# Optimization experiments

Hardware: AMD Instinct MI355X
Metric: run time of the kernel (lower is better)

## Reference

```python
import jax, jax.numpy as jnp
import numpy as np

B = 4096        # number of (drug, disease) pair graphs
N_PER = 60      # nodes per subgraph (>= k)
N = B * N_PER   # 245760 total nodes
E = 2_000_000   # edges
F_IN = 64
L1, L2 = 32, 32 # latent_dim
K = 30          # sort-pool k
N_DRUG, N_DIS = 1024, 2048


def gcn_conv(x, src, dst, W, b, n):
    # PyG GCNConv (eval): h = XW; symmetric norm with self-loops; out = A_hat h + b
    h = x @ W
    deg = jax.ops.segment_sum(jnp.ones(src.shape[0], h.dtype), dst, num_segments=n) + 1.0
    dinv = deg ** -0.5
    msg = h[src] * (dinv[src] * dinv[dst])[:, None]
    out = jax.ops.segment_sum(msg, dst, num_segments=n)
    out = out + h * (dinv * dinv)[:, None]  # self-loop contribution
    return out + b


def dense_gcn(x, adj, W, b):
    # PyG DenseGCNConv: set diag to 1, D^-1/2 A D^-1/2, out = A_hat (x W) + b
    n = adj.shape[0]
    eye = jnp.eye(n, dtype=adj.dtype)
    a = adj * (1.0 - eye) + eye
    deg = a.sum(-1)
    dinv = jnp.where(deg > 0, deg ** -0.5, 0.0)
    a = dinv[:, None] * a * dinv[None, :]
    return a @ (x @ W) + b


def conv1d(x, w, b, stride):
    out = jax.lax.conv_general_dilated(x, w, (stride,), 'VALID',
                                       dimension_numbers=('NCH', 'OIH', 'NCH'))
    return out + b[None, :, None]


def setup_inputs():
    key = jax.random.key(0)
    ks = jax.random.split(key, 24)
    x = jax.random.normal(ks[0], (N, F_IN), jnp.float32)
    edge_index = jax.random.randint(ks[1], (2, E), 0, N)
    batch = jnp.repeat(jnp.arange(B), N_PER)
    node = jnp.stack([jax.random.randint(ks[2], (B,), 0, N_DRUG),
                      jax.random.randint(ks[3], (B,), 0, N_DIS)], axis=1)
    di_sim = jax.random.normal(ks[4], (N_DRUG, N_DRUG), jnp.float32)
    dr_sim = jax.random.normal(ks[5], (N_DIS, N_DIS), jnp.float32)
    drug_adj = jax.random.uniform(ks[6], (N_DRUG, N_DRUG), jnp.float32)
    dis_adj = jax.random.uniform(ks[7], (N_DIS, N_DIS), jnp.float32)
    p = jnp.array(0.5, jnp.float32)

    def w(k, shape):
        return jax.random.normal(k, shape, jnp.float32) * 0.05

    z = lambda s: jnp.zeros(s, jnp.float32)
    params = dict(
        W1=w(ks[8], (F_IN, L1)), b1=z((L1,)),
        W2=w(ks[9], (L1, L2)), b2=z((L2,)),
        W3=w(ks[10], (256, 64)), b3=z((64,)),
        W4=w(ks[11], (64, 16)), b4=z((16,)),
        lin_di_w=w(ks[12], (N_DRUG, 256)), lin_di_b=z((256,)),
        lin_dr_w=w(ks[13], (N_DIS, 256)), lin_dr_b=z((256,)),
        c1_w=w(ks[14], (128, 1, L1 + L2)), c1_b=z((128,)),
        c2_w=w(ks[15], (256, 128, 5)), c2_b=z((256,)),
        lin1_w=w(ks[16], (2816, 128)), lin1_b=z((128,)),
        lin2_w=w(ks[17], (128, 32)), lin2_b=z((32,)),
        bn_g=jnp.ones((32,), jnp.float32), bn_b=z((32,)),
        fcs_w=w(ks[18], (64, 32)), fcs_b=z((32,)),
        fcs2_w=w(ks[19], (32, 1)), fcs2_b=z((1,)),
    )
    return dict(x=x, edge_index=edge_index, batch=batch, node=node,
                di_sim=di_sim, dr_sim=dr_sim, drug_adj=drug_adj,
                dis_adj=dis_adj, p=p, **params)


def reference(x, edge_index, batch, node, di_sim, dr_sim, drug_adj, dis_adj, p,
              W1, b1, W2, b2, W3, b3, W4, b4,
              lin_di_w, lin_di_b, lin_dr_w, lin_dr_b,
              c1_w, c1_b, c2_w, c2_b, lin1_w, lin1_b, lin2_w, lin2_b,
              bn_g, bn_b, fcs_w, fcs_b, fcs2_w, fcs2_b):
    src, dst = edge_index[0], edge_index[1]
    # two GCN layers over the pair subgraphs
    x1 = jax.nn.relu(gcn_conv(x, src, dst, W1, b1, N))
    x2 = jax.nn.relu(gcn_conv(x1, src, dst, W2, b2, N))
    cs = jnp.concatenate([x1, x2], axis=1)       # [N, 64]
    D = cs.shape[1]
    # sort-pool: equal-size graphs, batch contiguous -> reshape and sort per graph
    xb = cs.reshape(B, N_PER, D)
    order = jnp.argsort(-xb[:, :, -1], axis=-1)  # descending by last channel
    xs = jnp.take_along_axis(xb, order[:, :, None], axis=1)[:, :K]  # [B, K, D]
    h = xs.reshape(B, 1, K * D)
    h = jax.nn.relu(conv1d(h, c1_w, c1_b, D))    # [B, 128, K]
    h = jax.lax.reduce_window(h, -jnp.inf, jax.lax.max, (1, 1, 2), (1, 1, 2), 'VALID')
    h = jax.nn.relu(conv1d(h, c2_w, c2_b, 1))    # [B, 256, 11]
    h = h.reshape(B, -1)                         # [B, 2816]
    h = jax.nn.relu(h @ lin1_w + lin1_b)
    h = h @ lin2_w + lin2_b
    h = jax.nn.relu(h * bn_g + bn_b)             # BatchNorm eval (mean 0, var 1)
    # dense similarity-graph branches (conv3/conv4 weights shared across branches)
    di_e = di_sim @ lin_di_w + lin_di_b
    di_f = jax.nn.relu(dense_gcn(di_e, drug_adj, W3, b3))
    di_o = jax.nn.relu(dense_gcn(di_f, drug_adj, W4, b4))
    di = di_o[node[:, 0]]
    dr_e = dr_sim @ lin_dr_w + lin_dr_b
    dr_f = jax.nn.relu(dense_gcn(dr_e, dis_adj, W3, b3))
    dr_o = jax.nn.relu(dense_gcn(dr_f, dis_adj, W4, b4))
    dr = dr_o[node[:, 1]]
    feat = jnp.concatenate([di, dr], axis=1)     # [B, 32]
    z = jnp.concatenate([h * p, feat * (1.0 - p)], axis=1)  # [B, 64]
    z = jax.nn.relu(z @ fcs_w + fcs_b)
    return (z @ fcs2_w + fcs2_b)[:, 0]
```

## Files before the change

### kernel.cpp

```cpp
#include <hip/hip_runtime.h>

#define NN 245760
#define NB 4096
#define NPER 60
#define NE 2000000
#define KSEL 30
#define NDRUG 1024
#define NDIS 2048
#define NBKT 480
#define CHUNK 2048
#define SEGCAP 4992

typedef unsigned short ushort_t;
typedef unsigned int uint_t;
using bf16x8 = __attribute__((ext_vector_type(8))) short;
using f32x4 = __attribute__((ext_vector_type(4))) float;

__device__ inline ushort_t f2bf(float f) {
    union { float f; unsigned int u; } v; v.f = f;
    unsigned int r = v.u + 0x7FFF + ((v.u >> 16) & 1);
    return (ushort_t)(r >> 16);
}

__global__ __launch_bounds__(256) void k_bscatter(const int* __restrict__ ei,
                                                  int* __restrict__ bfill,
                                                  uint_t* __restrict__ pairs) {
    __shared__ int hist[NBKT], fill[NBKT], gbase[NBKT];
    int t = threadIdx.x;
    long e0 = (long)blockIdx.x * CHUNK;
    int cnt = (int)min((long)CHUNK, (long)NE - e0);
    for (int i = t; i < NBKT; i += 256) { hist[i] = 0; fill[i] = 0; }
    __syncthreads();
    for (int i = t; i < cnt; i += 256)
        atomicAdd(&hist[ei[NE + e0 + i] >> 9], 1);
    __syncthreads();
    for (int i = t; i < NBKT; i += 256)
        if (hist[i]) gbase[i] = i * SEGCAP + atomicAdd(&bfill[i], hist[i]);
    __syncthreads();
    for (int i = t; i < cnt; i += 256) {
        int s = ei[e0 + i], d = ei[NE + e0 + i];
        int b = d >> 9;
        int pos = gbase[b] + atomicAdd(&fill[b], 1);
        if (pos < (b + 1) * SEGCAP)
            pairs[pos] = ((uint_t)s << 9) | (uint_t)(d & 511);
    }
}

__global__ __launch_bounds__(256) void k_bbuild(const uint_t* __restrict__ pairs,
                                                const int* __restrict__ bfill,
                                                int* __restrict__ csr,
                                                int* __restrict__ rowp,
                                                int* __restrict__ cntg,
                                                float* __restrict__ dinv) {
    __shared__ int hist[512], nbase[512], nfill[512], scanA[512], scanB[512];
    __shared__ int seg[SEGCAP];
    int t = threadIdx.x, b = blockIdx.x;
    int ebase = b * SEGCAP;
    int ecnt = bfill[b];
    if (ecnt > SEGCAP) ecnt = SEGCAP;
    for (int i = t; i < 512; i += 256) { hist[i] = 0; nfill[i] = 0; }
    __syncthreads();
    for (int i = t; i < ecnt; i += 256)
        atomicAdd(&hist[pairs[ebase + i] & 511], 1);
    __syncthreads();
    for (int i = t; i < 512; i += 256) scanA[i] = hist[i];
    __syncthreads();
    int* src = scanA; int* dst = scanB;
    for (int off = 1; off < 512; off <<= 1) {
        for (int i = t; i < 512; i += 256)
            dst[i] = src[i] + ((i >= off) ? src[i - off] : 0);
        __syncthreads();
        int* tmp = src; src = dst; dst = tmp;
    }
    for (int i = t; i < 512; i += 256) {
        int h = hist[i];
        int excl = src[i] - h;
        nbase[i] = excl;
        int n = (b << 9) + i;
        rowp[n] = ebase + excl;
        cntg[n] = h;
        dinv[n] = 1.0f / sqrtf((float)h + 1.0f);
    }
    __syncthreads();
    for (int i = t; i < ecnt; i += 256) {
        uint_t v = pairs[ebase + i];
        int ln = v & 511;
        int pos = nbase[ln] + atomicAdd(&nfill[ln], 1);
        if (pos < SEGCAP) seg[pos] = (int)(v >> 9);
    }
    __syncthreads();
    for (int i = t; i < ecnt; i += 256) csr[ebase + i] = seg[i];
}

__global__ __launch_bounds__(256) void k_xw(const float* __restrict__ A, const float* __restrict__ W,
                                            float* __restrict__ h, int K, int lda) {
    __shared__ float Xs[64][65];
    __shared__ float Ws[64][32];
    int t = threadIdx.x;
    int r0 = blockIdx.x * 64;
    int kq = K >> 2;
    for (int idx = t; idx < 64 * kq; idx += 256) {
        int row = idx / kq, q = idx % kq;
        float4 v = *(const float4*)(A + (long)(r0 + row) * lda + q * 4);
        Xs[row][q * 4 + 0] = v.x; Xs[row][q * 4 + 1] = v.y;
        Xs[row][q * 4 + 2] = v.z; Xs[row][q * 4 + 3] = v.w;
    }
    for (int idx = t; idx < K * 32; idx += 256) ((float*)Ws)[idx] = W[idx];
    __syncthreads();
    int r = (t >> 3) * 2, c = (t & 7) * 4;
    float4 acc0 = {0, 0, 0, 0}, acc1 = {0, 0, 0, 0};
    for (int k = 0; k < K; k++) {
        float x0 = Xs[r][k], x1 = Xs[r + 1][k];
        float4 w = *(const float4*)&Ws[k][c];
        acc0.x += x0 * w.x; acc0.y += x0 * w.y; acc0.z += x0 * w.z; acc0.w += x0 * w.w;
        acc1.x += x1 * w.x; acc1.y += x1 * w.y; acc1.z += x1 * w.z; acc1.w += x1 * w.w;
    }
    *(float4*)(h + (long)(r0 + r) * 32 + c) = acc0;
    *(float4*)(h + (long)(r0 + r + 1) * 32 + c) = acc1;
}

__global__ void k_gcn_agg(const float* __restrict__ h, const int* __restrict__ csr,
                          const int* __restrict__ rowp, const int* __restrict__ cnt,
                          const float* __restrict__ dinv, const float* __restrict__ bias,
                          float* __restrict__ out, int colofs) {
    int t = threadIdx.x;
    int l = t & 7, g = t >> 3;
    int wl = t & 63;
    int gbase = wl & ~7;
    int d = blockIdx.x * 32 + g;
    float dd = dinv[d];
    int start = rowp[d], c = cnt[d];
    float4 hv = *(const float4*)(h + (long)d * 32 + l * 4);
    float4 acc; acc.x = dd * hv.x; acc.y = dd * hv.y; acc.z = dd * hv.z; acc.w = dd * hv.w;
    int k = 0;
    while (k < c) {
        int nb = c - k; if (nb > 8) nb = 8;
        int sl = (l < nb) ? csr[start + k + l] : 0;
        int sj[8]; float ds[8]; float4 hj[8];
#pragma unroll
        for (int j = 0; j < 8; j++)
            sj[j] = __shfl(sl, gbase + j, 64);
#pragma unroll
        for (int j = 0; j < 8; j++)
            if (j < nb) ds[j] = dinv[sj[j]];
#pragma unroll
        for (int j = 0; j < 8; j++)
            if (j < nb) hj[j] = *(const float4*)(h + (long)sj[j] * 32 + l * 4);
#pragma unroll
        for (int j = 0; j < 8; j++) {
            if (j < nb) {
                acc.x += ds[j] * hj[j].x;
                acc.y += ds[j] * hj[j].y;
                acc.z += ds[j] * hj[j].z;
                acc.w += ds[j] * hj[j].w;
            }
        }
        k += nb;
    }
    float4 bv = *(const float4*)(bias + l * 4);
    float* op = out + (long)d * 64 + colofs + l * 4;
    op[0] = fmaxf(dd * acc.x + bv.x, 0.f);
    op[1] = fmaxf(dd * acc.y + bv.y, 0.f);
    op[2] = fmaxf(dd * acc.z + bv.z, 0.f);
    op[3] = fmaxf(dd * acc.w + bv.w, 0.f);
}

__global__ __launch_bounds__(256, 2) void k_conv1_mfma(const float* __restrict__ cs,
                                                       const int* __restrict__ sel,
                                                       const ushort_t* __restrict__ c1w16,
                                                       const float* __restrict__ c1b,
                                                       ushort_t* __restrict__ po16) {
    __shared__ ushort_t A_lds[128 * 72];
    __shared__ ushort_t B_lds[128 * 72];
    int t = threadIdx.x;
    int r0 = blockIdx.x * 128;
#pragma unroll
    for (int rnd = 0; rnd < 4; rnd++) {
        int idx = t + rnd * 256;
        int row = idx >> 3, seg = idx & 7;
        const float* src = cs + (long)sel[r0 + row] * 64 + seg * 8;
        float4 v0 = *(const float4*)src;
        float4 v1 = *(const float4*)(src + 4);
        ushort_t tmp[8] = {f2bf(v0.x), f2bf(v0.y), f2bf(v0.z), f2bf(v0.w),
                           f2bf(v1.x), f2bf(v1.y), f2bf(v1.z), f2bf(v1.w)};
        *(uint4*)&A_lds[row * 72 + seg * 8] = *(uint4*)tmp;
        *(uint4*)&B_lds[row * 72 + seg * 8] = *(const uint4*)(c1w16 + row * 64 + seg * 8);
    }
    __syncthreads();
    int wv = t >> 6, lane = t & 63;
    int wm = wv >> 1, wn = wv & 1;
    int lrow = lane & 15, lk = (lane >> 4) * 8, lr4 = (lane >> 4) * 4;
    f32x4 acc[4][4] = {};
#pragma unroll
    for (int kk = 0; kk < 2; kk++) {
        bf16x8 a[4], b[4];
#pragma unroll
        for (int f = 0; f < 4; f++) {
            a[f] = *(const bf16x8*)&A_lds[(wm * 64 + f * 16 + lrow) * 72 + kk * 32 + lk];
            b[f] = *(const bf16x8*)&B_lds[(wn * 64 + f * 16 + lrow) * 72 + kk * 32 + lk];
        }
#pragma unroll
        for (int i = 0; i < 4; i++)
#pragma unroll
            for (int j = 0; j < 4; j++)
                acc[i][j] = __builtin_amdgcn_mfma_f32_16x16x32_bf16(a[i], b[j], acc[i][j], 0, 0, 0);
    }
    __syncthreads();
    ushort_t* po_lds = A_lds;
#pragma unroll
    for (int fn = 0; fn < 4; fn++) {
        int col = wn * 64 + fn * 16 + lrow;
        float bb = c1b[col];
#pragma unroll
        for (int fm = 0; fm < 4; fm++) {
            int lrow2 = wm * 32 + fm * 8 + (lr4 >> 1);
            float v0 = fmaxf(acc[fm][fn][0] + bb, 0.f);
            float v1 = fmaxf(acc[fm][fn][1] + bb, 0.f);
            float v2 = fmaxf(acc[fm][fn][2] + bb, 0.f);
            float v3 = fmaxf(acc[fm][fn][3] + bb, 0.f);
            po_lds[lrow2 * 128 + col]       = f2bf(fmaxf(v0, v1));
            po_lds[(lrow2 + 1) * 128 + col] = f2bf(fmaxf(v2, v3));
        }
    }
    __syncthreads();
    uint4* dst = (uint4*)(po16 + (long)(r0 >> 1) * 128);
    const uint4* srcp = (const uint4*)po_lds;
#pragma unroll
    for (int i = 0; i < 4; i++) dst[t + i * 256] = srcp[t + i * 256];
}

__global__ __launch_bounds__(256, 2) void k_conv2_mfma(const ushort_t* __restrict__ pool16,
                                                       const ushort_t* __restrict__ w2colT,
                                                       ushort_t* __restrict__ act2,
                                                       const float* __restrict__ bias) {
    __shared__ ushort_t smem[2 * 128 * 72];
    ushort_t* A_lds = smem;
    ushort_t* B_lds = smem + 128 * 72;
    int t = threadIdx.x;
    int r0 = blockIdx.x * 128, c0 = blockIdx.y * 128;
    long abase[4]; const ushort_t* bptr[4]; int lofs[4];
#pragma unroll
    for (int rnd = 0; rnd < 4; rnd++) {
        int idx = t + rnd * 256;
        int row = idx >> 3, seg = idx & 7;
        int arow = r0 + row;
        int bb = arow / 11, tt2 = arow - bb * 11;
        abase[rnd] = (long)(bb * 15 + tt2) * 128 + seg * 8;
        bptr[rnd] = w2colT + (long)(c0 + row) * 640 + seg * 8;
        lofs[rnd] = row * 72 + seg * 8;
    }
    int wv = t >> 6, lane = t & 63;
    int wm = wv >> 1, wn = wv & 1;
    int lrow = lane & 15, lk = (lane >> 4) * 8, lr4 = (lane >> 4) * 4;
    f32x4 acc[4][4] = {};
    for (int k0 = 0; k0 < 640; k0 += 64) {
#pragma unroll
        for (int rnd = 0; rnd < 4; rnd++) {
            *(uint4*)&A_lds[lofs[rnd]] = *(const uint4*)(pool16 + abase[rnd] + k0);
            *(uint4*)&B_lds[lofs[rnd]] = *(const uint4*)(bptr[rnd] + k0);
        }
        __syncthreads();
#pragma unroll
        for (int kk = 0; kk < 2; kk++) {
            bf16x8 a[4], b[4];
#pragma unroll
            for (int f = 0; f < 4; f++) {
                a[f] = *(const bf16x8*)&A_lds[(wm * 64 + f * 16 + lrow) * 72 + kk * 32 + lk];
                b[f] = *(const bf16x8*)&B_lds[(wn * 64 + f * 16 + lrow) * 72 + kk * 32 + lk];
            }
#pragma unroll
            for (int i = 0; i < 4; i++)
#pragma unroll
                for (int j = 0; j < 4; j++)
                    acc[i][j] = __builtin_amdgcn_mfma_f32_16x16x32_bf16(a[i], b[j], acc[i][j], 0, 0, 0);
        }
        __syncthreads();
    }
    ushort_t* c_lds = smem;
#pragma unroll
    for (int fn = 0; fn < 4; fn++) {
        int col = wn * 64 + fn * 16 + lrow;
        float bv = bias[c0 + col];
#pragma unroll
        for (int fm = 0; fm < 4; fm++) {
            int lr = wm * 64 + fm * 16 + lr4;
#pragma unroll
            for (int j = 0; j < 4; j++)
                c_lds[(lr + j) * 128 + col] = f2bf(fmaxf(acc[fm][fn][j] + bv, 0.f));
        }
    }
    __syncthreads();
#pragma unroll
    for (int i = 0; i < 8; i++) {
        int idx = t + i * 256;
        int row = idx >> 4, q = idx & 15;
        *(uint4*)(act2 + (long)(r0 + row) * 256 + c0 + q * 8) = ((const uint4*)c_lds)[idx];
    }
}

__global__ __launch_bounds__(256, 2) void k_lin1_mfma(const ushort_t* __restrict__ A,
                                                      const ushort_t* __restrict__ Bm,
                                                      float* __restrict__ C) {
    __shared__ ushort_t A_lds[128 * 72];
    __shared__ ushort_t B_lds[128 * 72];
    int t = threadIdx.x;
    int r0 = blockIdx.x * 128;
    int kz = blockIdx.z;
    const ushort_t* ap[4]; const ushort_t* bp[4]; int lofs[4];
#pragma unroll
    for (int rnd = 0; rnd < 4; rnd++) {
        int idx = t + rnd * 256;
        int row = idx >> 3, seg = idx & 7;
        ap[rnd] = A + (long)(r0 + row) * 2816 + kz * 704 + seg * 8;
        bp[rnd] = Bm + (long)row * 2816 + kz * 704 + seg * 8;
        lofs[rnd] = row * 72 + seg * 8;
    }
    int wv = t >> 6, lane = t & 63;
    int wm = wv >> 1, wn = wv & 1;
    int lrow = lane & 15, lk = (lane >> 4) * 8, lr4 = (lane >> 4) * 4;
    f32x4 acc[4][4] = {};
    for (int k0 = 0; k0 < 704; k0 += 64) {
#pragma unroll
        for (int rnd = 0; rnd < 4; rnd++) {
            *(uint4*)&A_lds[lofs[rnd]] = *(const uint4*)(ap[rnd] + k0);
            *(uint4*)&B_lds[lofs[rnd]] = *(const uint4*)(bp[rnd] + k0);
        }
        __syncthreads();
#pragma unroll
        for (int kk = 0; kk < 2; kk++) {
            bf16x8 a[4], b[4];
#pragma unroll
            for (int f = 0; f < 4; f++) {
                a[f] = *(const bf16x8*)&A_lds[(wm * 64 + f * 16 + lrow) * 72 + kk * 32 + lk];
                b[f] = *(const bf16x8*)&B_lds[(wn * 64 + f * 16 + lrow) * 72 + kk * 32 + lk];
            }
#pragma unroll
            for (int i = 0; i < 4; i++)
#pragma unroll
                for (int j = 0; j < 4; j++)
                    acc[i][j] = __builtin_amdgcn_mfma_f32_16x16x32_bf16(a[i], b[j], acc[i][j], 0, 0, 0);
        }
        __syncthreads();
    }
#pragma unroll
    for (int fn = 0; fn < 4; fn++) {
        int col = wn * 64 + fn * 16 + lrow;
#pragma unroll
        for (int fm = 0; fm < 4; fm++) {
            int rowb = r0 + wm * 64 + fm * 16 + lr4;
#pragma unroll
            for (int j = 0; j < 4; j++)
                atomicAdd(&C[(long)(rowb + j) * 128 + col], acc[fm][fn][j]);
        }
    }
}

__global__ __launch_bounds__(256, 2) void k_de_mfma(
    const ushort_t* __restrict__ A0, const ushort_t* __restrict__ B0, float* __restrict__ C0,
    const float* __restrict__ bias0, int M0, int K0, int KS0,
    const ushort_t* __restrict__ A1, const ushort_t* __restrict__ B1, float* __restrict__ C1,
    const float* __restrict__ bias1, int M1, int K1, int KS1) {
    __shared__ ushort_t A_lds[128 * 72];
    __shared__ ushort_t B_lds[64 * 72];
    int z = blockIdx.z;
    const ushort_t* A; const ushort_t* Bm; float* C; const float* bias; int M, K, kz, KS;
    if (z < KS0) { A = A0; Bm = B0; C = C0; bias = bias0; M = M0; K = K0; kz = z; KS = KS0; }
    else { A = A1; Bm = B1; C = C1; bias = bias1; M = M1; K = K1; kz = z - KS0; KS = KS1; }
    int r0 = blockIdx.x * 128, c0 = blockIdx.y * 64;
    if (r0 >= M) return;
    int Kc = K / KS;
    int kb = kz * Kc;
    int t = threadIdx.x;
    const ushort_t* ap[4]; int alofs[4];
#pragma unroll
    for (int rnd = 0; rnd < 4; rnd++) {
        int idx = t + rnd * 256;
        int row = idx >> 3, seg = idx & 7;
        ap[rnd] = A + (long)(r0 + row) * K + kb + seg * 8;
        alofs[rnd] = row * 72 + seg * 8;
    }
    const ushort_t* bp[2]; int blofs[2];
#pragma unroll
    for (int rnd = 0; rnd < 2; rnd++) {
        int idx = t + rnd * 256;
        int row = idx >> 3, seg = idx & 7;
        bp[rnd] = Bm + (long)(c0 + row) * K + kb + seg * 8;
        blofs[rnd] = row * 72 + seg * 8;
    }
    int wv = t >> 6, lane = t & 63;
    int lrow = lane & 15, lk = (lane >> 4) * 8, lr4 = (lane >> 4) * 4;
    uint4 areg[4], breg[2];
#pragma unroll
    for (int rnd = 0; rnd < 4; rnd++) areg[rnd] = *(const uint4*)(ap[rnd]);
#pragma unroll
    for (int rnd = 0; rnd < 2; rnd++) breg[rnd] = *(const uint4*)(bp[rnd]);
    f32x4 acc[2][4] = {};
    for (int k0 = 0; k0 < Kc; k0 += 64) {
#pragma unroll
        for (int rnd = 0; rnd < 4; rnd++) *(uint4*)&A_lds[alofs[rnd]] = areg[rnd];
#pragma unroll
        for (int rnd = 0; rnd < 2; rnd++) *(uint4*)&B_lds[blofs[rnd]] = breg[rnd];
        __syncthreads();
        if (k0 + 64 < Kc) {
#pragma unroll
            for (int rnd = 0; rnd < 4; rnd++) areg[rnd] = *(const uint4*)(ap[rnd] + k0 + 64);
#pragma unroll
            for (int rnd = 0; rnd < 2; rnd++) breg[rnd] = *(const uint4*)(bp[rnd] + k0 + 64);
        }
#pragma unroll
        for (int kk = 0; kk < 2; kk++) {
            bf16x8 a[2], b[4];
#pragma unroll
            for (int f = 0; f < 2; f++)
                a[f] = *(const bf16x8*)&A_lds[(wv * 32 + f * 16 + lrow) * 72 + kk * 32 + lk];
#pragma unroll
            for (int f = 0; f < 4; f++)
                b[f] = *(const bf16x8*)&B_lds[(f * 16 + lrow) * 72 + kk * 32 + lk];
#pragma unroll
            for (int i = 0; i < 2; i++)
#pragma unroll
                for (int j = 0; j < 4; j++)
                    acc[i][j] = __builtin_amdgcn_mfma_f32_16x16x32_bf16(a[i], b[j], acc[i][j], 0, 0, 0);
        }
        __syncthreads();
    }
#pragma unroll
    for (int fn = 0; fn < 4; fn++) {
        int col = c0 + fn * 16 + lrow;
        float bv = (kz == 0) ? bias[col] : 0.f;
#pragma unroll
        for (int fm = 0; fm < 2; fm++) {
            int rowb = r0 + wv * 32 + fm * 16 + lr4;
#pragma unroll
            for (int j = 0; j < 4; j++)
                atomicAdd(&C[(long)(rowb + j) * 256 + col], acc[fm][fn][j] + bv);
        }
    }
}

__global__ __launch_bounds__(256, 2) void k_g_mfma(
    const ushort_t* __restrict__ A0, const ushort_t* __restrict__ B0, float* __restrict__ C0,
    int M0, int K0, int KS0,
    const ushort_t* __restrict__ A1, const ushort_t* __restrict__ B1, float* __restrict__ C1,
    int M1, int K1, int KS1) {
    __shared__ ushort_t A_lds[128 * 72];
    __shared__ ushort_t B_lds[64 * 72];
    int z = blockIdx.z;
    const ushort_t* A; const ushort_t* Bm; float* C; int M, K, kz, KS;
    if (z < KS0) { A = A0; Bm = B0; C = C0; M = M0; K = K0; kz = z; KS = KS0; }
    else { A = A1; Bm = B1; C = C1; M = M1; K = K1; kz = z - KS0; KS = KS1; }
    int r0 = blockIdx.x * 128;
    if (r0 >= M) return;
    int Kc = K / KS;
    int kb = kz * Kc;
    int t = threadIdx.x;
    const ushort_t* ap[4]; int alofs[4];
#pragma unroll
    for (int rnd = 0; rnd < 4; rnd++) {
        int idx = t + rnd * 256;
        int row = idx >> 3, seg = idx & 7;
        ap[rnd] = A + (long)(r0 + row) * K + kb + seg * 8;
        alofs[rnd] = row * 72 + seg * 8;
    }
    const ushort_t* bp[2]; int blofs[2];
#pragma unroll
    for (int rnd = 0; rnd < 2; rnd++) {
        int idx = t + rnd * 256;
        int row = idx >> 3, seg = idx & 7;
        bp[rnd] = Bm + (long)row * K + kb + seg * 8;
        blofs[rnd] = row * 72 + seg * 8;
    }
    int wv = t >> 6, lane = t & 63;
    int lrow = lane & 15, lk = (lane >> 4) * 8, lr4 = (lane >> 4) * 4;
    uint4 areg[4], breg[2];
#pragma unroll
    for (int rnd = 0; rnd < 4; rnd++) areg[rnd] = *(const uint4*)(ap[rnd]);
#pragma unroll
    for (int rnd = 0; rnd < 2; rnd++) breg[rnd] = *(const uint4*)(bp[rnd]);
    f32x4 acc[2][4] = {};
    for (int k0 = 0; k0 < Kc; k0 += 64) {
#pragma unroll
        for (int rnd = 0; rnd < 4; rnd++) *(uint4*)&A_lds[alofs[rnd]] = areg[rnd];
#pragma unroll
        for (int rnd = 0; rnd < 2; rnd++) *(uint4*)&B_lds[blofs[rnd]] = breg[rnd];
        __syncthreads();
        if (k0 + 64 < Kc) {
#pragma unroll
            for (int rnd = 0; rnd < 4; rnd++) areg[rnd] = *(const uint4*)(ap[rnd] + k0 + 64);
#pragma unroll
            for (int rnd = 0; rnd < 2; rnd++) breg[rnd] = *(const uint4*)(bp[rnd] + k0 + 64);
        }
#pragma unroll
        for (int kk = 0; kk < 2; kk++) {
            bf16x8 a[2], b[4];
#pragma unroll
            for (int f = 0; f < 2; f++)
                a[f] = *(const bf16x8*)&A_lds[(wv * 32 + f * 16 + lrow) * 72 + kk * 32 + lk];
#pragma unroll
            for (int f = 0; f < 4; f++)
                b[f] = *(const bf16x8*)&B_lds[(f * 16 + lrow) * 72 + kk * 32 + lk];
#pragma unroll
            for (int i = 0; i < 2; i++)
#pragma unroll
                for (int j = 0; j < 4; j++)
                    acc[i][j] = __builtin_amdgcn_mfma_f32_16x16x32_bf16(a[i], b[j], acc[i][j], 0, 0, 0);
        }
        __syncthreads();
    }
#pragma unroll
    for (int fn = 0; fn < 4; fn++) {
        int col = fn * 16 + lrow;
#pragma unroll
        for (int fm = 0; fm < 2; fm++) {
            int rowb = r0 + wv * 32 + fm * 16 + lr4;
#pragma unroll
            for (int j = 0; j < 4; j++)
                atomicAdd(&C[(long)(rowb + j) * 64 + col], acc[fm][fn][j]);
        }
    }
}

__global__ void k_cvt2(const float* __restrict__ a0, ushort_t* __restrict__ o0, long n0,
                       const float* __restrict__ a1, ushort_t* __restrict__ o1, long n1) {
    long i4 = ((long)blockIdx.x * 256 + threadIdx.x) * 4;
    const float* a; ushort_t* o;
    if (i4 < n0) { a = a0 + i4; o = o0 + i4; }
    else {
        long j = i4 - n0;
        if (j >= n1) return;
        a = a1 + j; o = o1 + j;
    }
    float4 v = *(const float4*)a;
    o[0] = f2bf(v.x); o[1] = f2bf(v.y); o[2] = f2bf(v.z); o[3] = f2bf(v.w);
}

__global__ void k_linwT2(const float* __restrict__ w0, ushort_t* __restrict__ o0, int K0,
                         const float* __restrict__ w1, ushort_t* __restrict__ o1, int K1) {
    __shared__ float tile[64][65];
    int nb0 = K0 / 64;
    int bx = blockIdx.x;
    const float* w; ushort_t* o; int K, kt;
    if (bx < nb0) { w = w0; o = o0; K = K0; kt = bx; }
    else { w = w1; o = o1; K = K1; kt = bx - nb0; }
    int n0 = blockIdx.y * 64, k0 = kt * 64;
    int t = threadIdx.x;
    int r = t >> 6, c = t & 63;
    for (int rr = r; rr < 64; rr += 4)
        tile[rr][c] = w[(long)(k0 + rr) * 256 + n0 + c];
    __syncthreads();
    for (int rr = r; rr < 64; rr += 4)
        o[(long)(n0 + rr) * K + k0 + c] = f2bf(tile[c][rr]);
}

__global__ void k_uT2(const float* __restrict__ u0, ushort_t* __restrict__ o0, int K0,
                      const float* __restrict__ u1, ushort_t* __restrict__ o1, int K1) {
    __shared__ float tile[64][65];
    int nb0 = K0 / 64;
    int bx = blockIdx.x;
    const float* u; ushort_t* o; int K, kt;
    if (bx < nb0) { u = u0; o = o0; K = K0; kt = bx; }
    else { u = u1; o = o1; K = K1; kt = bx - nb0; }
    int k0 = kt * 64;
    int t = threadIdx.x;
    int r = t >> 6, c = t & 63;
    for (int rr = r; rr < 64; rr += 4)
        tile[rr][c] = u[(long)(k0 + rr) * 64 + c];
    __syncthreads();
    for (int rr = r; rr < 64; rr += 4)
        o[(long)rr * K + k0 + c] = f2bf(tile[c][rr]);
}

__global__ __launch_bounds__(256) void k_gemm_sk(
    const float* A0, const float* B0, float* C0, const float* ab0p, const float* cs0p,
    int M0, int N0, int K0, int lda0, int KS0, int Kc0,
    const float* A1, const float* B1, float* C1, const float* ab1p, const float* cs1p,
    int M1, int N1, int K1, int lda1, int KS1, int Kc1) {
    int z = blockIdx.z;
    const float* A; const float* Bm; float* C; const float* abp; const float* csp;
    int M, N, K, lda, kz, Kc;
    if (z < KS0) { A = A0; Bm = B0; C = C0; abp = ab0p; csp = cs0p; M = M0; N = N0; K = K0; lda = lda0; kz = z; Kc = Kc0; }
    else { A = A1; Bm = B1; C = C1; abp = ab1p; csp = cs1p; M = M1; N = N1; K = K1; lda = lda1; kz = z - KS0; Kc = Kc1; }
    int r0 = blockIdx.x * 64, c0 = blockIdx.y * 64;
    if (r0 >= M || c0 >= N) return;
    int kb = kz * Kc, ke = min(K, kb + Kc);
    __shared__ float As[16][68];
    __shared__ float Bs[16][68];
    int t = threadIdx.x;
    int tx = t & 15, ty = t >> 4;
    float acc[4][4] = {};
    int ar = t >> 2, aq = (t & 3) * 4;
    long abase = (long)(r0 + ar) * lda;
    int brow = t >> 4, bc = (t & 15) * 4;
    float4 av = *(const float4*)(A + abase + kb + aq);
    if (abp) {
        float4 abv = *(const float4*)(abp + kb + aq);
        av.x += abv.x; av.y += abv.y; av.z += abv.z; av.w += abv.w;
    }
    float4 bv = *(const float4*)(Bm + (long)(kb + brow) * N + c0 + bc);
    for (int k0 = kb; k0 < ke; k0 += 16) {
        As[aq + 0][ar] = av.x; As[aq + 1][ar] = av.y; As[aq + 2][ar] = av.z; As[aq + 3][ar] = av.w;
        *(float4*)&Bs[brow][bc] = bv;
        __syncthreads();
        if (k0 + 16 < ke) {
            av = *(const float4*)(A + abase + k0 + 16 + aq);
            if (abp) {
                float4 abv = *(const float4*)(abp + k0 + 16 + aq);
                av.x += abv.x; av.y += abv.y; av.z += abv.z; av.w += abv.w;
            }
            bv = *(const float4*)(Bm + (long)(k0 + 16 + brow) * N + c0 + bc);
        }
#pragma unroll
        for (int kk = 0; kk < 16; kk++) {
            float4 a4 = *(const float4*)&As[kk][ty * 4];
            float4 b4 = *(const float4*)&Bs[kk][tx * 4];
            float aa[4] = {a4.x, a4.y, a4.z, a4.w};
            float bb2[4] = {b4.x, b4.y, b4.z, b4.w};
#pragma unroll
            for (int i = 0; i < 4; i++)
#pragma unroll
                for (int j = 0; j < 4; j++) acc[i][j] += aa[i] * bb2[j];
        }
        __syncthreads();
    }
#pragma unroll
    for (int i = 0; i < 4; i++) {
        int row = r0 + ty * 4 + i;
        float sc = csp ? csp[row] : 1.0f;
#pragma unroll
        for (int j = 0; j < 4; j++)
            atomicAdd(&C[(long)row * N + c0 + tx * 4 + j], acc[i][j] * sc);
    }
}

__global__ void k_dense_deg2(const float* __restrict__ adj0, float* __restrict__ d0, int n0,
                             const float* __restrict__ adj1, float* __restrict__ d1, int n1) {
    int lane = threadIdx.x & 63;
    int row = (blockIdx.x * blockDim.x + threadIdx.x) >> 6;
    const float* adj; float* dv; int n, r;
    if (row < n0) { adj = adj0; dv = d0; n = n0; r = row; }
    else {
        r = row - n0;
        if (r >= n1) return;
        adj = adj1; dv = d1; n = n1;
    }
    const float* rp = adj + (long)r * n;
    float s = 0.f;
    for (int j = lane; j < n; j += 64) s += rp[j];
    for (int off = 32; off > 0; off >>= 1) s += __shfl_down(s, off, 64);
    if (lane == 0) {
        float deg = s - rp[r] + 1.0f;
        dv[r] = (deg > 0.f) ? 1.0f / sqrtf(deg) : 0.f;
    }
}

__global__ void k_fix_w4(const float* g0, const float* u0, const float* adj0, const float* d0, float* o0, int n0,
                         const float* g1, const float* u1, const float* adj1, const float* d1, float* o1, int n1,
                         const float* __restrict__ b3, const float* __restrict__ W4) {
    __shared__ float dfs[16][68];
    __shared__ float W4s[64 * 16];
    int t = threadIdx.x;
    for (int i = t; i < 1024; i += 256) W4s[i] = W4[i];
    int bx = blockIdx.x, nb0 = n0 / 16;
    const float* g; const float* u; const float* adj; const float* dv; float* o; int n, r0;
    if (bx < nb0) { g = g0; u = u0; adj = adj0; dv = d0; o = o0; n = n0; r0 = bx * 16; }
    else { g = g1; u = u1; adj = adj1; dv = d1; o = o1; n = n1; r0 = (bx - nb0) * 16; }
    int r = t >> 4;
    int row = r0 + r;
    float di = dv[row];
    float om = 1.0f - adj[(long)row * n + row];
    int c4 = (t & 15) * 4;
    float4 gv = *(const float4*)(g + (long)row * 64 + c4);
    float4 uv = *(const float4*)(u + (long)row * 64 + c4);
    float4 bv = *(const float4*)(b3 + c4);
    dfs[r][c4 + 0] = fmaxf(di * (gv.x + om * uv.x) + bv.x, 0.f);
    dfs[r][c4 + 1] = fmaxf(di * (gv.y + om * uv.y) + bv.y, 0.f);
    dfs[r][c4 + 2] = fmaxf(di * (gv.z + om * uv.z) + bv.z, 0.f);
    dfs[r][c4 + 3] = fmaxf(di * (gv.w + om * uv.w) + bv.w, 0.f);
    __syncthreads();
    int c = t & 15;
    float accv = 0.f;
#pragma unroll
    for (int k = 0; k < 64; k++) accv += dfs[r][k] * W4s[k * 16 + c];
    o[row * 16 + c] = di * accv;
}

__global__ void k_fixup2(const float* g0, const float* t0, const float* adj0, const float* d0, float* C0, long n0,
                         const float* g1, const float* t1, const float* adj1, const float* d1, float* C1, long n1,
                         const float* bias, int cols) {
    long idx = (long)blockIdx.x * 256 + threadIdx.x;
    long s0 = n0 * cols;
    const float* g; const float* tt; const float* adj; const float* dv; float* C; long n, li;
    if (idx < s0) { g = g0; tt = t0; adj = adj0; dv = d0; C = C0; n = n0; li = idx; }
    else {
        li = idx - s0;
        if (li >= n1 * cols) return;
        g = g1; tt = t1; adj = adj1; dv = d1; C = C1; n = n1;
    }
    long i = li / cols; int j = li % cols;
    float v = dv[i] * (g[li] + (1.0f - adj[i * n + i]) * tt[li]) + bias[j];
    C[li] = fmaxf(v, 0.f);
}

__global__ void k_adj16(const float* adj0, const float* u0, float* C0, int n0, int KS0, int Kc0,
                        const float* adj1, const float* u1, float* C1, int n1, int KS1, int Kc1) {
    int z = blockIdx.z;
    const float* adj; const float* u; float* C; int n, kz, Kc;
    if (z < KS0) { adj = adj0; u = u0; C = C0; n = n0; kz = z; Kc = Kc0; }
    else { adj = adj1; u = u1; C = C1; n = n1; kz = z - KS0; Kc = Kc1; }
    int r0 = blockIdx.x * 16;
    if (r0 >= n) return;
    int t = threadIdx.x;
    int r = r0 + (t >> 4), c = t & 15;
    int kb = kz * Kc, ke = min(n, kb + Kc);
    const float* arp = adj + (long)r * n;
    float acc = 0.f;
    for (int k = kb; k < ke; k += 4) {
        float4 a = *(const float4*)(arp + k);
        acc += a.x * u[(k + 0) * 16 + c] + a.y * u[(k + 1) * 16 + c]
             + a.z * u[(k + 2) * 16 + c] + a.w * u[(k + 3) * 16 + c];
    }
    atomicAdd(&C[r * 16 + c], acc);
}

__global__ void k_select(const float* __restrict__ cs, int* __restrict__ sel) {
    __shared__ float kk[240];
    int t = threadIdx.x;
    int b0 = blockIdx.x * 4;
    if (t < 240) kk[t] = cs[((long)(b0 * 60 + t)) * 64 + 63];
    __syncthreads();
    if (t < 240) {
        int lb = t / 60, i = t % 60;
        float key = kk[lb * 60 + i];
        int r = 0;
        for (int j = 0; j < 60; j++) {
            float kj = kk[lb * 60 + j];
            r += (kj > key) || (kj == key && j < i);
        }
        if (r < KSEL) sel[(b0 + lb) * KSEL + r] = (b0 + lb) * 60 + i;
    }
}

__global__ void k_w2colT(const float* __restrict__ c2w, ushort_t* __restrict__ o) {
    int idx = blockIdx.x * blockDim.x + threadIdx.x;
    if (idx >= 256 * 640) return;
    int oc = idx / 640, q = idx % 640;
    int tap = q >> 7, ic = q & 127;
    o[idx] = f2bf(c2w[(oc * 128 + ic) * 5 + tap]);
}

__global__ void k_w1pT(const float* __restrict__ w, ushort_t* __restrict__ o) {
    int idx = blockIdx.x * blockDim.x + threadIdx.x;
    if (idx >= 128 * 2816) return;
    int j = idx / 2816, c = idx % 2816;
    int tt = c >> 8, oc = c & 255;
    o[idx] = f2bf(w[(oc * 11 + tt) * 128 + j]);
}

__global__ void k_lin2_bn(const float* __restrict__ x, const float* __restrict__ l1b,
                          const float* __restrict__ w,
                          const float* __restrict__ b, const float* __restrict__ g,
                          const float* __restrict__ bb, float* __restrict__ o) {
    int t = blockIdx.x * blockDim.x + threadIdx.x;
    int j = t & 31, bi = t >> 5;
    const float* xr = x + (long)bi * 128;
    float acc = b[j];
    for (int k = 0; k < 128; k++) acc += fmaxf(xr[k] + l1b[k], 0.f) * w[k * 32 + j];
    o[bi * 32 + j] = fmaxf(acc * g[j] + bb[j], 0.f);
}

__global__ __launch_bounds__(256) void k_final(const float* __restrict__ hfin, const int* __restrict__ node,
                                               const float* __restrict__ dio, const float* __restrict__ dro,
                                               const float* __restrict__ pp,
                                               const float* __restrict__ fw, const float* __restrict__ fb,
                                               const float* __restrict__ f2w, const float* __restrict__ f2b,
                                               float* __restrict__ out) {
    __shared__ float w[64 * 32];
    __shared__ float w2[32];
    int t = threadIdx.x;
    for (int f = t; f < 2048; f += 256) w[f] = fw[f];
    if (t < 32) w2[t] = f2w[t];
    __syncthreads();
    int b = blockIdx.x * 256 + t;
    float p = *pp, q = 1.0f - p;
    float zin[64];
#pragma unroll
    for (int i = 0; i < 32; i++) zin[i] = hfin[b * 32 + i] * p;
    int n0 = node[b * 2], n1 = node[b * 2 + 1];
#pragma unroll
    for (int i = 0; i < 16; i++) zin[32 + i] = dio[n0 * 16 + i] * q;
#pragma unroll
    for (int i = 0; i < 16; i++) zin[48 + i] = dro[n1 * 16 + i] * q;
    float res = f2b[0];
    for (int j = 0; j < 32; j++) {
        float acc = fb[j];
#pragma unroll
        for (int i = 0; i < 64; i++) acc += zin[i] * w[i * 32 + j];
        res += fmaxf(acc, 0.f) * w2[j];
    }
    out[b] = res;
}

extern "C" void kernel_launch(void* const* d_in, const int* in_sizes, int n_in,
                              void* d_out, int out_size, void* d_ws, size_t ws_size,
                              hipStream_t stream) {
    const float* x        = (const float*)d_in[0];
    const int*   ei       = (const int*)d_in[1];
    const int*   node     = (const int*)d_in[3];
    const float* di_sim   = (const float*)d_in[4];
    const float* dr_sim   = (const float*)d_in[5];
    const float* drug_adj = (const float*)d_in[6];
    const float* dis_adj  = (const float*)d_in[7];
    const float* p        = (const float*)d_in[8];
    const float* W1 = (const float*)d_in[9],  *b1 = (const float*)d_in[10];
    const float* W2 = (const float*)d_in[11], *b2 = (const float*)d_in[12];
    const float* W3 = (const float*)d_in[13], *b3 = (const float*)d_in[14];
    const float* W4 = (const float*)d_in[15], *b4 = (const float*)d_in[16];
    const float* lin_di_w = (const float*)d_in[17], *lin_di_b = (const float*)d_in[18];
    const float* lin_dr_w = (const float*)d_in[19], *lin_dr_b = (const float*)d_in[20];
    const float* c1w = (const float*)d_in[21], *c1b = (const float*)d_in[22];
    const float* c2w = (const float*)d_in[23], *c2b = (const float*)d_in[24];
    const float* lin1w = (const float*)d_in[25], *lin1b = (const float*)d_in[26];
    const float* lin2w = (const float*)d_in[27], *lin2b = (const float*)d_in[28];
    const float* bng = (const float*)d_in[29], *bnb = (const float*)d_in[30];
    const float* fcsw = (const float*)d_in[31], *fcsb = (const float*)d_in[32];
    const float* fcs2w = (const float*)d_in[33], *fcs2b = (const float*)d_in[34];

    char* ws = (char*)d_ws;
    size_t o = 0;
    auto alloc = [&](size_t bytes) { size_t r = o; o += (bytes + 255) & ~(size_t)255; return r; };
    int*   csr     = (int*)(ws + alloc((size_t)NBKT * SEGCAP * 4));
    int*   rowp    = (int*)(ws + alloc((size_t)NN * 4));
    int*   degcnt  = (int*)(ws + alloc((size_t)NN * 4));
    float* dinvn   = (float*)(ws + alloc((size_t)NN * 4));
    float* hbuf    = (float*)(ws + alloc((size_t)NN * 32 * 4));
    float* cs      = (float*)(ws + alloc((size_t)NN * 64 * 4));
    int*   sel     = (int*)(ws + alloc((size_t)NB * KSEL * 4));
    float* hfin    = (float*)(ws + alloc((size_t)NB * 32 * 4));
    ushort_t* w2colT = (ushort_t*)(ws + alloc((size_t)256 * 640 * 2));
    ushort_t* w1pT   = (ushort_t*)(ws + alloc((size_t)128 * 2816 * 2));
    float* ddin_di = (float*)(ws + alloc((size_t)NDRUG * 4));
    float* ddin_dr = (float*)(ws + alloc((size_t)NDIS * 4));
    float* dt2_di  = (float*)(ws + alloc((size_t)NDRUG * 16 * 4));
    float* dt2_dr  = (float*)(ws + alloc((size_t)NDIS * 16 * 4));
    float* do_di   = (float*)(ws + alloc((size_t)NDRUG * 16 * 4));
    float* do_dr   = (float*)(ws + alloc((size_t)NDIS * 16 * 4));
    size_t zbase = o;
    int*   bfill   = (int*)(ws + alloc((size_t)NBKT * 4));
    float* lin1o   = (float*)(ws + alloc((size_t)NB * 128 * 4));
    float* de_di   = (float*)(ws + alloc((size_t)NDRUG * 256 * 4));
    float* de_dr   = (float*)(ws + alloc((size_t)NDIS * 256 * 4));
    float* dt_di   = (float*)(ws + alloc((size_t)NDRUG * 64 * 4));
    float* dt_dr   = (float*)(ws + alloc((size_t)NDIS * 64 * 4));
    float* dg_di   = (float*)(ws + alloc((size_t)NDRUG * 64 * 4));
    float* dg_dr   = (float*)(ws + alloc((size_t)NDIS * 64 * 4));
    float* dg2_di  = (float*)(ws + alloc((size_t)NDRUG * 16 * 4));
    float* dg2_dr  = (float*)(ws + alloc((size_t)NDIS * 16 * 4));
    size_t zsize = o - zbase;
    uint_t* pairsg   = (uint_t*)cs;
    ushort_t* pool16 = (ushort_t*)hbuf;
    ushort_t* act2   = (ushort_t*)cs;
    char* hb = (char*)hbuf;
    ushort_t* di_sim16 = (ushort_t*)(hb + 15728640);
    ushort_t* dr_sim16 = (ushort_t*)(hb + 17825792);
    ushort_t* lindiT16 = (ushort_t*)(hb + 26214400);
    ushort_t* lindrT16 = (ushort_t*)(hb + 26738688);
    ushort_t* c1w16    = (ushort_t*)(hb + 27787264);
    ushort_t* uT16_di  = (ushort_t*)(hb + 27811840);
    ushort_t* uT16_dr  = (ushort_t*)(hb + 27942912);
    ushort_t* drugadj16 = di_sim16;
    ushort_t* disadj16  = dr_sim16;

    hipMemsetAsync(ws + zbase, 0, zsize, stream);

    k_bscatter<<<(NE + CHUNK - 1) / CHUNK, 256, 0, stream>>>(ei, bfill, pairsg);
    k_bbuild<<<NBKT, 256, 0, stream>>>(pairsg, bfill, csr, rowp, degcnt, dinvn);

    k_xw<<<NN / 64, 256, 0, stream>>>(x, W1, hbuf, 64, 64);
    k_gcn_agg<<<NN / 32, 256, 0, stream>>>(hbuf, csr, rowp, degcnt, dinvn, b1, cs, 0);
    k_xw<<<NN / 64, 256, 0, stream>>>(cs, W2, hbuf, 32, 64);
    k_gcn_agg<<<NN / 32, 256, 0, stream>>>(hbuf, csr, rowp, degcnt, dinvn, b2, cs, 32);

    k_select<<<NB / 4, 256, 0, stream>>>(cs, sel);

    k_cvt2<<<5120, 256, 0, stream>>>(di_sim, di_sim16, (long)NDRUG * NDRUG,
                                     dr_sim, dr_sim16, (long)NDIS * NDIS);
    k_linwT2<<<dim3(48, 4), 256, 0, stream>>>(lin_di_w, lindiT16, NDRUG,
                                              lin_dr_w, lindrT16, NDIS);
    k_de_mfma<<<dim3(16, 4, 12), 256, 0, stream>>>(
        di_sim16, lindiT16, de_di, lin_di_b, NDRUG, NDRUG, 4,
        dr_sim16, lindrT16, de_dr, lin_dr_b, NDIS, NDIS, 8);
    k_dense_deg2<<<(NDRUG + NDIS) * 64 / 256, 256, 0, stream>>>(drug_adj, ddin_di, NDRUG, dis_adj, ddin_dr, NDIS);
    k_cvt2<<<5120, 256, 0, stream>>>(drug_adj, drugadj16, (long)NDRUG * NDRUG,
                                     dis_adj, disadj16, (long)NDIS * NDIS);

    k_cvt2<<<8, 256, 0, stream>>>(c1w, c1w16, 8192, c1w, c1w16, 0);
    k_w2colT<<<(256 * 640 + 255) / 256, 256, 0, stream>>>(c2w, w2colT);
    k_w1pT<<<(128 * 2816 + 255) / 256, 256, 0, stream>>>(lin1w, w1pT);

    k_conv1_mfma<<<960, 256, 0, stream>>>(cs, sel, c1w16, c1b, pool16);

    k_conv2_mfma<<<dim3(352, 2), 256, 0, stream>>>(pool16, w2colT, act2, c2b);

    k_lin1_mfma<<<dim3(32, 1, 4), 256, 0, stream>>>(act2, w1pT, lin1o);
    k_lin2_bn<<<NB * 32 / 256, 256, 0, stream>>>(lin1o, lin1b, lin2w, lin2b, bng, bnb, hfin);

    k_gemm_sk<<<dim3(NDIS / 64, 1, 8), 256, 0, stream>>>(
        de_di, W3, dt_di, nullptr, ddin_di, NDRUG, 64, 256, 256, 4, 64,
        de_dr, W3, dt_dr, nullptr, ddin_dr, NDIS, 64, 256, 256, 4, 64);
    k_uT2<<<48, 256, 0, stream>>>(dt_di, uT16_di, NDRUG, dt_dr, uT16_dr, NDIS);
    k_g_mfma<<<dim3(16, 1, 24), 256, 0, stream>>>(
        drugadj16, uT16_di, dg_di, NDRUG, NDRUG, 8,
        disadj16, uT16_dr, dg_dr, NDIS, NDIS, 16);
    k_fix_w4<<<(NDRUG + NDIS) / 16, 256, 0, stream>>>(
        dg_di, dt_di, drug_adj, ddin_di, dt2_di, NDRUG,
        dg_dr, dt_dr, dis_adj, ddin_dr, dt2_dr, NDIS, b3, W4);
    k_adj16<<<dim3(NDIS / 16, 1, 6), 256, 0, stream>>>(
        drug_adj, dt2_di, dg2_di, NDRUG, 2, 512,
        dis_adj, dt2_dr, dg2_dr, NDIS, 4, 512);
    k_fixup2<<<((NDRUG + NDIS) * 16 + 255) / 256, 256, 0, stream>>>(
        dg2_di, dt2_di, drug_adj, ddin_di, do_di, NDRUG,
        dg2_dr, dt2_dr, dis_adj, ddin_dr, do_dr, NDIS, b4, 16);

    k_final<<<NB / 256, 256, 0, stream>>>(hfin, node, do_di, do_dr, p, fcsw, fcsb, fcs2w, fcs2b, (float*)d_out);
}
```

Before: 462.3 us.

## Replace two-pass bucketed CSR build with fixed-capacity per-node slot scatter

Replaces the two-kernel bucket scatter and per-bucket CSR build with a single kernel that uses a global atomic per destination node and writes sources into fixed slots of DCAP=32 per node. A small kernel then computes dinv from the counts. This drops the shared-memory histogram, scan and compaction passes and the intermediate pairs buffer. In exchange it issues 2M global atomics scattered over 245K counters, uses a larger padded CSR array, and silently drops edges past 32 per node. With average in-degree around 8 that cap should rarely be hit, but neighbour order is now nondeterministic.

New measurement: 517.9 us. +12.0%, slower.

```diff
diff --git a/kernel.cpp b/kernel.cpp
--- a/kernel.cpp
+++ b/kernel.cpp
@@ -7,9 +7,7 @@
 #define KSEL 30
 #define NDRUG 1024
 #define NDIS 2048
-#define NBKT 480
-#define CHUNK 2048
-#define SEGCAP 4992
+#define DCAP 32
 
 typedef unsigned short ushort_t;
 typedef unsigned int uint_t;
@@ -22,74 +20,21 @@
     return (ushort_t)(r >> 16);
 }
 
-__global__ __launch_bounds__(256) void k_bscatter(const int* __restrict__ ei,
-                                                  int* __restrict__ bfill,
-                                                  uint_t* __restrict__ pairs) {
-    __shared__ int hist[NBKT], fill[NBKT], gbase[NBKT];
-    int t = threadIdx.x;
-    long e0 = (long)blockIdx.x * CHUNK;
-    int cnt = (int)min((long)CHUNK, (long)NE - e0);
-    for (int i = t; i < NBKT; i += 256) { hist[i] = 0; fill[i] = 0; }
-    __syncthreads();
-    for (int i = t; i < cnt; i += 256)
-        atomicAdd(&hist[ei[NE + e0 + i] >> 9], 1);
-    __syncthreads();
-    for (int i = t; i < NBKT; i += 256)
-        if (hist[i]) gbase[i] = i * SEGCAP + atomicAdd(&bfill[i], hist[i]);
-    __syncthreads();
-    for (int i = t; i < cnt; i += 256) {
-        int s = ei[e0 + i], d = ei[NE + e0 + i];
-        int b = d >> 9;
-        int pos = gbase[b] + atomicAdd(&fill[b], 1);
-        if (pos < (b + 1) * SEGCAP)
-            pairs[pos] = ((uint_t)s << 9) | (uint_t)(d & 511);
-    }
-}
-
-__global__ __launch_bounds__(256) void k_bbuild(const uint_t* __restrict__ pairs,
-                                                const int* __restrict__ bfill,
-                                                int* __restrict__ csr,
-                                                int* __restrict__ rowp,
-                                                int* __restrict__ cntg,
-                                                float* __restrict__ dinv) {
-    __shared__ int hist[512], nbase[512], nfill[512], scanA[512], scanB[512];
-    __shared__ int seg[SEGCAP];
-    int t = threadIdx.x, b = blockIdx.x;
-    int ebase = b * SEGCAP;
-    int ecnt = bfill[b];
-    if (ecnt > SEGCAP) ecnt = SEGCAP;
-    for (int i = t; i < 512; i += 256) { hist[i] = 0; nfill[i] = 0; }
-    __syncthreads();
-    for (int i = t; i < ecnt; i += 256)
-        atomicAdd(&hist[pairs[ebase + i] & 511], 1);
-    __syncthreads();
-    for (int i = t; i < 512; i += 256) scanA[i] = hist[i];
-    __syncthreads();
-    int* src = scanA; int* dst = scanB;
-    for (int off = 1; off < 512; off <<= 1) {
-        for (int i = t; i < 512; i += 256)
-            dst[i] = src[i] + ((i >= off) ? src[i - off] : 0);
-        __syncthreads();
-        int* tmp = src; src = dst; dst = tmp;
-    }
-    for (int i = t; i < 512; i += 256) {
-        int h = hist[i];
-        int excl = src[i] - h;
-        nbase[i] = excl;
-        int n = (b << 9) + i;
-        rowp[n] = ebase + excl;
-        cntg[n] = h;
-        dinv[n] = 1.0f / sqrtf((float)h + 1.0f);
-    }
-    __syncthreads();
-    for (int i = t; i < ecnt; i += 256) {
-        uint_t v = pairs[ebase + i];
-        int ln = v & 511;
-        int pos = nbase[ln] + atomicAdd(&nfill[ln], 1);
-        if (pos < SEGCAP) seg[pos] = (int)(v >> 9);
-    }
-    __syncthreads();
-    for (int i = t; i < ecnt; i += 256) csr[ebase + i] = seg[i];
+__global__ __launch_bounds__(256) void k_edge_scatter(const int* __restrict__ ei,
+                                                      int* __restrict__ cnt,
+                                                      int* __restrict__ csr) {
+    int idx = blockIdx.x * 256 + threadIdx.x;
+    int stride = gridDim.x * 256;
+    for (int e = idx; e < NE; e += stride) {
+        int s = ei[e], d = ei[NE + e];
+        int pos = atomicAdd(&cnt[d], 1);
+        if (pos < DCAP) csr[(long)d * DCAP + pos] = s;
+    }
+}
+
+__global__ void k_dinv(const int* __restrict__ cnt, float* __restrict__ dinv) {
+    int n = blockIdx.x * 256 + threadIdx.x;
+    if (n < NN) dinv[n] = 1.0f / sqrtf((float)cnt[n] + 1.0f);
 }
 
 __global__ __launch_bounds__(256) void k_xw(const float* __restrict__ A, const float* __restrict__ W,
@@ -120,7 +65,7 @@
 }
 
 __global__ void k_gcn_agg(const float* __restrict__ h, const int* __restrict__ csr,
-                          const int* __restrict__ rowp, const int* __restrict__ cnt,
+                          const int* __restrict__ cnt,
                           const float* __restrict__ dinv, const float* __restrict__ bias,
                           float* __restrict__ out, int colofs) {
     int t = threadIdx.x;
@@ -129,7 +74,8 @@
     int gbase = wl & ~7;
     int d = blockIdx.x * 32 + g;
     float dd = dinv[d];
-    int start = rowp[d], c = cnt[d];
+    int start = d * DCAP;
+    int c = cnt[d]; if (c > DCAP) c = DCAP;
     float4 hv = *(const float4*)(h + (long)d * 32 + l * 4);
     float4 acc; acc.x = dd * hv.x; acc.y = dd * hv.y; acc.z = dd * hv.z; acc.w = dd * hv.w;
     int k = 0;
@@ -828,9 +774,7 @@
     char* ws = (char*)d_ws;
     size_t o = 0;
     auto alloc = [&](size_t bytes) { size_t r = o; o += (bytes + 255) & ~(size_t)255; return r; };
-    int*   csr     = (int*)(ws + alloc((size_t)NBKT * SEGCAP * 4));
-    int*   rowp    = (int*)(ws + alloc((size_t)NN * 4));
-    int*   degcnt  = (int*)(ws + alloc((size_t)NN * 4));
+    int*   csr     = (int*)(ws + alloc((size_t)NN * DCAP * 4));
     float* dinvn   = (float*)(ws + alloc((size_t)NN * 4));
     float* hbuf    = (float*)(ws + alloc((size_t)NN * 32 * 4));
     float* cs      = (float*)(ws + alloc((size_t)NN * 64 * 4));
@@ -845,7 +789,7 @@
     float* do_di   = (float*)(ws + alloc((size_t)NDRUG * 16 * 4));
     float* do_dr   = (float*)(ws + alloc((size_t)NDIS * 16 * 4));
     size_t zbase = o;
-    int*   bfill   = (int*)(ws + alloc((size_t)NBKT * 4));
+    int*   degcnt  = (int*)(ws + alloc((size_t)NN * 4));
     float* lin1o   = (float*)(ws + alloc((size_t)NB * 128 * 4));
     float* de_di   = (float*)(ws + alloc((size_t)NDRUG * 256 * 4));
     float* de_dr   = (float*)(ws + alloc((size_t)NDIS * 256 * 4));
@@ -856,7 +800,6 @@
     float* dg2_di  = (float*)(ws + alloc((size_t)NDRUG * 16 * 4));
     float* dg2_dr  = (float*)(ws + alloc((size_t)NDIS * 16 * 4));
     size_t zsize = o - zbase;
-    uint_t* pairsg   = (uint_t*)cs;
     ushort_t* pool16 = (ushort_t*)hbuf;
     ushort_t* act2   = (ushort_t*)cs;
     char* hb = (char*)hbuf;
@@ -872,13 +815,13 @@
 
     hipMemsetAsync(ws + zbase, 0, zsize, stream);
 
-    k_bscatter<<<(NE + CHUNK - 1) / CHUNK, 256, 0, stream>>>(ei, bfill, pairsg);
-    k_bbuild<<<NBKT, 256, 0, stream>>>(pairsg, bfill, csr, rowp, degcnt, dinvn);
+    k_edge_scatter<<<2048, 256, 0, stream>>>(ei, degcnt, csr);
+    k_dinv<<<(NN + 255) / 256, 256, 0, stream>>>(degcnt, dinvn);
 
     k_xw<<<NN / 64, 256, 0, stream>>>(x, W1, hbuf, 64, 64);
-    k_gcn_agg<<<NN / 32, 256, 0, stream>>>(hbuf, csr, rowp, degcnt, dinvn, b1, cs, 0);
+    k_gcn_agg<<<NN / 32, 256, 0, stream>>>(hbuf, csr, degcnt, dinvn, b1, cs, 0);
     k_xw<<<NN / 64, 256, 0, stream>>>(cs, W2, hbuf, 32, 64);
-    k_gcn_agg<<<NN / 32, 256, 0, stream>>>(hbuf, csr, rowp, degcnt, dinvn, b2, cs, 32);
+    k_gcn_agg<<<NN / 32, 256, 0, stream>>>(hbuf, csr, degcnt, dinvn, b2, cs, 32);
 
     k_select<<<NB / 4, 256, 0, stream>>>(cs, sel);
 
```
